# Kernel optimization log

Measured on AMD Instinct MI355X. Metric: run time of the kernel, lower is better.

The kernel has to match this reference:

```python
import jax, jax.numpy as jnp
import numpy as np

B, C, O, N, T, K = 4, 64, 64, 32768, 4, 9
PAD, DIL = 4, 1  # padding*dilation, dilation
SIGMA = 0.05
EPS_BN = 1e-5


def _gather_ch(x, idx):
    # x: [B, C, N], idx: [B, N] -> gather along last dim per channel
    idx3 = jnp.broadcast_to(idx[:, None, :], x.shape)
    return jnp.take_along_axis(x, idx3, axis=-1)


def _weighted_conv(x, coords, w):
    # x: [B,C,N], coords: [B,3,N], w: [O,C,K]
    xp = jnp.pad(x, ((0, 0), (0, 0), (PAD, PAD)))
    cp = jnp.pad(coords, ((0, 0), (0, 0), (PAD, PAD)))
    win_idx = jnp.arange(N)[:, None] + jnp.arange(K) * DIL  # [N, K]
    win = xp[:, :, win_idx]   # [B,C,N,K]
    cwin = cp[:, :, win_idx]  # [B,3,N,K]
    d = cwin - cwin[:, :, :, K // 2:K // 2 + 1]
    s = jnp.sum(d * d, axis=1)                    # [B,N,K]
    r = jnp.sqrt(jnp.where(s > 0, s, 1.0))
    r = jnp.where(s > 0, r, 0.0)
    wgt = jnp.maximum(1.0 - r / SIGMA, 0.0)       # [B,N,K]
    return jnp.einsum('bcnk,bnk,ock->bon', win, wgt, w)


def _bn(x, g, b):
    # training-mode BatchNorm1d over (B, N)
    m = jnp.mean(x, axis=(0, 2), keepdims=True)
    v = jnp.var(x, axis=(0, 2), keepdims=True)
    return g[None, :, None] * (x - m) * jax.lax.rsqrt(v + EPS_BN) + b[None, :, None]


def setup_inputs() -> dict:
    key = jax.random.key(0)
    ks = jax.random.split(key, 12)
    inp = jax.random.normal(ks[0], (B, C, N), dtype=jnp.float32)
    # coords in a small box so sigma=0.05 yields non-trivial weights
    multi_coords = jax.random.uniform(ks[1], (B, 3, N, T), dtype=jnp.float32) * 0.02
    indices = jax.random.randint(ks[2], (B, N, T), 0, N, dtype=jnp.int32)
    reindices = jax.random.randint(ks[3], (B, N, T), 0, N, dtype=jnp.int32)
    fan = C * K
    conv_w = jax.random.normal(ks[4], (T, O, C, K), dtype=jnp.float32) / np.sqrt(fan)
    bn_gamma = jnp.ones((T, O), dtype=jnp.float32)
    bn_beta = jnp.zeros((T, O), dtype=jnp.float32)
    fusion_w = jax.random.normal(ks[5], (O, T * O), dtype=jnp.float32) / np.sqrt(T * O)
    fusion_b = jnp.zeros((O,), dtype=jnp.float32)
    fusion_gamma = jnp.ones((O,), dtype=jnp.float32)
    fusion_beta = jnp.zeros((O,), dtype=jnp.float32)
    return {"input": inp, "multi_coords": multi_coords, "indices": indices,
            "reindices": reindices, "conv_w": conv_w, "bn_gamma": bn_gamma,
            "bn_beta": bn_beta, "fusion_w": fusion_w, "fusion_b": fusion_b,
            "fusion_gamma": fusion_gamma, "fusion_beta": fusion_beta}


def reference(input, multi_coords, indices, reindices, conv_w, bn_gamma, bn_beta,
              fusion_w, fusion_b, fusion_gamma, fusion_beta):
    outs = []
    for i in range(T):  # fixed small set of 4 Hilbert orders
        x = _gather_ch(input, indices[:, :, i])            # [B,C,N]
        x = _weighted_conv(x, multi_coords[:, :, :, i], conv_w[i])  # [B,O,N]
        x = _bn(x, bn_gamma[i], bn_beta[i])
        x = _gather_ch(x, reindices[:, :, i])
        outs.append(x)
    cat = jnp.concatenate(outs, axis=1)                    # [B, T*O, N]
    y = jnp.einsum('bcn,oc->bon', cat, fusion_w) + fusion_b[None, :, None]
    y = _bn(y, fusion_gamma, fusion_beta)
    return jax.nn.relu(y)
```

## Files before the change

kernel.cpp:

```cpp
#include <hip/hip_runtime.h>
#include <hip/hip_bf16.h>

#define BB 4
#define CC 64
#define OO 64
#define NN 32768
#define TT 4
#define KK 9
#define PADW 4
#define SIGMA 0.05f
#define EPS_BN 1e-5f

typedef __attribute__((ext_vector_type(8))) short bf16x8;
typedef __attribute__((ext_vector_type(4))) float f32x4;

__device__ __forceinline__ unsigned short f2bf(float f) {
  __hip_bfloat16 h = __float2bfloat16(f);
  return *reinterpret_cast<unsigned short*>(&h);
}
__device__ __forceinline__ float bf2f(unsigned short u) {
  unsigned int x = ((unsigned int)u) << 16;
  float f;
  __builtin_memcpy(&f, &x, 4);
  return f;
}
__device__ __forceinline__ unsigned int pkbf(float a, float b) {
  float2 t; t.x = a; t.y = b;
  __hip_bfloat162 h = __float22bfloat162_rn(t);
  unsigned int r;
  __builtin_memcpy(&r, &h, 4);
  return r;
}

__global__ __launch_bounds__(256) void transpose_kernel(
    const float* __restrict__ inp, unsigned short* __restrict__ xTb)
{
  const int n0 = blockIdx.x * 64;
  const int b  = blockIdx.y;
  const int tid = threadIdx.x;
  __shared__ float xt[64][65];
  {
    int nl = tid & 63, c4 = tid >> 6;
    #pragma unroll
    for (int i = 0; i < 16; ++i) {
      int c = c4 * 16 + i;
      xt[c][nl] = inp[((size_t)(b*CC + c))*NN + n0 + nl];
    }
  }
  __syncthreads();
  {
    int nl = tid >> 2, cq = tid & 3;
    unsigned int pk[8];
    #pragma unroll
    for (int i = 0; i < 8; ++i) {
      int c = cq*16 + i*2;
      pk[i] = pkbf(xt[c][nl], xt[c+1][nl]);
    }
    unsigned int* dst = (unsigned int*)(xTb + (((size_t)b*NN) + n0 + nl)*CC + cq*16);
    ((int4*)dst)[0] = make_int4((int)pk[0],(int)pk[1],(int)pk[2],(int)pk[3]);
    ((int4*)dst)[1] = make_int4((int)pk[4],(int)pk[5],(int)pk[6],(int)pk[7]);
  }
}

__global__ __launch_bounds__(256) void wprep_kernel(
    const float* __restrict__ cw, unsigned short* __restrict__ W4)
{
  const int k = blockIdx.x;
  const int t = blockIdx.y;
  for (int u = threadIdx.x; u < OO*CC; u += 256) {
    int o = u >> 6, c = u & 63;
    int ow = o >> 5, ot = (o >> 4) & 1, l15 = o & 15;
    int frag = c >> 5, q = (c >> 3) & 3, j = c & 7;
    float wv = cw[(((size_t)(t*OO + o))*CC + c)*KK + k];
    W4[(size_t)(t*9+k)*4096 + ow*2048 + ot*1024 + frag*512 + l15*32 + q*8 + j]
        = f2bf(wv);
  }
}

__global__ __launch_bounds__(256, 6) void conv_kernel(
    const unsigned short* __restrict__ xTb,
    const float* __restrict__ mc,
    const int*   __restrict__ ind,
    const unsigned short* __restrict__ W4,
    unsigned short* __restrict__ Y,
    float* __restrict__ cpart2)
{
  const int n0  = blockIdx.x * 128;
  const int b   = blockIdx.y;
  const int t   = blockIdx.z;
  const int tid = threadIdx.x;
  const int lane = tid & 63;
  const int w    = tid >> 6;
  const int l15  = lane & 15;
  const int q    = lane >> 4;
  const int ow   = w & 1;
  const int nw   = w >> 1;

  __shared__ short xg[136][72];
  __shared__ float wgl[128][10];
  __shared__ float mcs[3][140];

  int4 g[5];
  #pragma unroll
  for (int i = 0; i < 5; ++i) {
    int u = tid + 256*i;
    g[i] = make_int4(0,0,0,0);
    if (u < 1088) {
      int p = u >> 3, s = u & 7;
      int m = n0 + p - PADW;
      if (m >= 0 && m < NN) {
        int idx = ind[((size_t)b*NN + m)*TT + t];
        g[i] = *(const int4*)(xTb + ((size_t)b*NN + idx)*CC + s*8);
      }
    }
  }

  if (tid < 136) {
    int m = n0 + tid - PADW;
    #pragma unroll
    for (int d = 0; d < 3; ++d) {
      float4 v = make_float4(0.f, 0.f, 0.f, 0.f);
      if (m >= 0 && m < NN)
        v = *(const float4*)(mc + (((size_t)(b*3+d))*NN + m)*TT);
      mcs[d][tid] = (t==0) ? v.x : (t==1) ? v.y : (t==2) ? v.z : v.w;
    }
  }

  #pragma unroll
  for (int i = 0; i < 5; ++i) {
    int u = tid + 256*i;
    if (u < 1088) {
      int p = u >> 3, s = u & 7;
      *(int4*)&xg[p][s*8] = g[i];
    }
  }
  __syncthreads();

  {
    int nl = tid >> 1;
    int k0 = (tid & 1) * 5;
    int kc = 5 - (tid & 1);
    float cx = mcs[0][nl+4], cy = mcs[1][nl+4], cz = mcs[2][nl+4];
    for (int i2 = 0; i2 < kc; ++i2) {
      int k = k0 + i2, mi = nl + k;
      float dx = mcs[0][mi]-cx, dy = mcs[1][mi]-cy, dz = mcs[2][mi]-cz;
      float s2 = dx*dx + dy*dy + dz*dz;
      float r = (s2 > 0.f) ? sqrtf(s2) : 0.f;
      wgl[nl][k] = fmaxf(1.f - r*(1.f/SIGMA), 0.f);
    }
  }
  __syncthreads();

  const unsigned short* Wt = W4 + (size_t)t*9*4096 + ow*2048 + (l15*4 + q)*8;
  const f32x4 Z = {0.f, 0.f, 0.f, 0.f};
  f32x4 fin[2][4];
  #pragma unroll
  for (int ot = 0; ot < 2; ++ot)
    #pragma unroll
    for (int ns = 0; ns < 4; ++ns) fin[ot][ns] = Z;

  for (int k = 0; k < KK; ++k) {
    const unsigned short* Wk = Wt + (size_t)k*4096;
    bf16x8 af[2][2];
    #pragma unroll
    for (int ot = 0; ot < 2; ++ot) {
      af[ot][0] = *(const bf16x8*)(Wk + ot*1024);
      af[ot][1] = *(const bf16x8*)(Wk + ot*1024 + 512);
    }
    #pragma unroll
    for (int ns = 0; ns < 4; ++ns) {
      int nl = nw*64 + ns*16 + l15;
      int p  = nl + k;
      bf16x8 b0 = *(const bf16x8*)&xg[p][q*8];
      bf16x8 b1 = *(const bf16x8*)&xg[p][32 + q*8];
      float wgt = wgl[nl][k];
      #pragma unroll
      for (int ot = 0; ot < 2; ++ot) {
        f32x4 d = __builtin_amdgcn_mfma_f32_16x16x32_bf16(af[ot][0], b0, Z, 0, 0, 0);
        d = __builtin_amdgcn_mfma_f32_16x16x32_bf16(af[ot][1], b1, d, 0, 0, 0);
        fin[ot][ns] += wgt * d;
      }
    }
  }

  #pragma unroll
  for (int ns = 0; ns < 4; ++ns) {
    int nl = nw*64 + ns*16 + l15;
    size_t row = (((size_t)t*BB + b)*NN + n0 + nl)*OO;
    #pragma unroll
    for (int ot = 0; ot < 2; ++ot) {
      uint2 pk2;
      pk2.x = pkbf(fin[ot][ns][0], fin[ot][ns][1]);
      pk2.y = pkbf(fin[ot][ns][2], fin[ot][ns][3]);
      *(uint2*)(Y + row + ow*32 + ot*16 + q*4) = pk2;
    }
  }

  float sv[16];
  #pragma unroll
  for (int ot = 0; ot < 2; ++ot)
    #pragma unroll
    for (int r = 0; r < 4; ++r) {
      float a = 0.f, qs = 0.f;
      #pragma unroll
      for (int ns = 0; ns < 4; ++ns) {
        float v = fin[ot][ns][r];
        a += v; qs += v*v;
      }
      sv[ot*4+r] = a; sv[8+ot*4+r] = qs;
    }
  #pragma unroll
  for (int msk = 1; msk < 16; msk <<= 1) {
    #pragma unroll
    for (int i = 0; i < 16; ++i) sv[i] += __shfl_xor(sv[i], msk, 16);
  }
  if (l15 == 0) {
    int slot4 = ((b*256 + (int)blockIdx.x) << 2) | w;
    #pragma unroll
    for (int ot = 0; ot < 2; ++ot)
      #pragma unroll
      for (int r = 0; r < 4; ++r) {
        int o = ow*32 + ot*16 + q*4 + r;
        cpart2[((size_t)((t*64 + o)*2 + 0))*4096 + slot4] = sv[ot*4+r];
        cpart2[((size_t)((t*64 + o)*2 + 1))*4096 + slot4] = sv[8+ot*4+r];
      }
  }
}

__global__ __launch_bounds__(256) void bnparam_kernel(
    const float* __restrict__ cpart2,
    const float* __restrict__ gam,
    const float* __restrict__ bet,
    float* __restrict__ ss)
{
  const int to = blockIdx.x;
  const int tid = threadIdx.x;
  __shared__ float r1[256], r2[256];
  const float* p1 = cpart2 + (size_t)to*2*4096;
  const float* p2 = p1 + 4096;
  float s1 = 0.f, s2 = 0.f;
  for (int i = tid*4; i < 4096; i += 1024) {
    float4 a = *(const float4*)(p1 + i);
    float4 c = *(const float4*)(p2 + i);
    s1 += a.x + a.y + a.z + a.w;
    s2 += c.x + c.y + c.z + c.w;
  }
  r1[tid] = s1; r2[tid] = s2;
  __syncthreads();
  for (int st = 128; st > 0; st >>= 1) {
    if (tid < st) { r1[tid] += r1[tid+st]; r2[tid] += r2[tid+st]; }
    __syncthreads();
  }
  if (tid == 0) {
    const float inv = 1.f / (float)(BB * NN);
    float mean = r1[0] * inv;
    float var  = r2[0] * inv - mean * mean;
    float sc = gam[to] * rsqrtf(var + EPS_BN);
    ss[to*2 + 0] = sc;
    ss[to*2 + 1] = bet[to] - mean * sc;
  }
}

__global__ __launch_bounds__(256, 6) void fusion_kernel(
    const unsigned short* __restrict__ Y,
    const int*   __restrict__ rind,
    const float* __restrict__ ss,
    const float* __restrict__ fw,
    const float* __restrict__ fb,
    float* __restrict__ out,
    float* __restrict__ fpart2)
{
  const int n0  = blockIdx.x * 128;
  const int b   = blockIdx.y;
  const int tid = threadIdx.x;
  const int lane = tid & 63;
  const int w    = tid >> 6;
  const int l15  = lane & 15;
  const int q    = lane >> 4;
  const int ow   = w & 1;
  const int nw   = w >> 1;

  __shared__ short zg[128][72];
  __shared__ int   rnl[TT][128];
  __shared__ float ssl[512];

  for (int u = tid; u < 512; u += 256) {
    int tt = u >> 7, nl = u & 127;
    rnl[tt][nl] = rind[((size_t)b*NN + n0 + nl)*TT + tt];
  }
  ssl[tid]       = ss[tid];
  ssl[tid + 256] = ss[tid + 256];
  __syncthreads();

  f32x4 fin[2][4];
  #pragma unroll
  for (int ot = 0; ot < 2; ++ot)
    #pragma unroll
    for (int ns = 0; ns < 4; ++ns) fin[ot][ns] = (f32x4){0.f,0.f,0.f,0.f};

  for (int r = 0; r < 4; ++r) {
    if (r) __syncthreads();
    #pragma unroll
    for (int i = 0; i < 4; ++i) {
      int u = tid + 256*i;
      int n = u >> 3, s = u & 7;
      int rn = rnl[r][n];
      int4 raw = *(const int4*)(Y + (((size_t)r*BB + b)*NN + rn)*OO + s*8);
      const unsigned short* rp = (const unsigned short*)&raw;
      int cb = r*64 + s*8;
      unsigned int pk[4];
      #pragma unroll
      for (int j = 0; j < 4; ++j) {
        float v0 = bf2f(rp[2*j  ]) * ssl[(cb+2*j  )*2] + ssl[(cb+2*j  )*2+1];
        float v1 = bf2f(rp[2*j+1]) * ssl[(cb+2*j+1)*2] + ssl[(cb+2*j+1)*2+1];
        pk[j] = pkbf(v0, v1);
      }
      *(int4*)&zg[n][s*8] = make_int4((int)pk[0],(int)pk[1],(int)pk[2],(int)pk[3]);
    }
    __syncthreads();

    #pragma unroll
    for (int kk = 0; kk < 2; ++kk) {
      bf16x8 af[2];
      #pragma unroll
      for (int ot = 0; ot < 2; ++ot) {
        const float* wp = fw + (size_t)(ow*32 + ot*16 + l15)*256 + r*64 + kk*32 + q*8;
        float4 wa = *(const float4*)wp;
        float4 wb = *(const float4*)(wp + 4);
        unsigned int u0 = pkbf(wa.x, wa.y), u1 = pkbf(wa.z, wa.w);
        unsigned int u2 = pkbf(wb.x, wb.y), u3 = pkbf(wb.z, wb.w);
        int4 tmp = make_int4((int)u0,(int)u1,(int)u2,(int)u3);
        __builtin_memcpy(&af[ot], &tmp, 16);
      }
      #pragma unroll
      for (int ns = 0; ns < 4; ++ns) {
        int nl = nw*64 + ns*16 + l15;
        bf16x8 bfr = *(const bf16x8*)&zg[nl][kk*32 + q*8];
        #pragma unroll
        for (int ot = 0; ot < 2; ++ot)
          fin[ot][ns] = __builtin_amdgcn_mfma_f32_16x16x32_bf16(af[ot], bfr, fin[ot][ns], 0, 0, 0);
      }
    }
  }

  float sv[16];
  #pragma unroll
  for (int ot = 0; ot < 2; ++ot)
    #pragma unroll
    for (int rr = 0; rr < 4; ++rr) {
      int o = ow*32 + ot*16 + q*4 + rr;
      float bias = fb[o];
      float* dst = out + ((size_t)(b*OO + o))*NN + n0 + nw*64;
      float a = 0.f, qs = 0.f;
      #pragma unroll
      for (int ns = 0; ns < 4; ++ns) {
        float v = fin[ot][ns][rr] + bias;
        dst[ns*16 + l15] = v;
        a += v; qs += v*v;
      }
      sv[ot*4+rr] = a; sv[8+ot*4+rr] = qs;
    }
  #pragma unroll
  for (int msk = 1; msk < 16; msk <<= 1) {
    #pragma unroll
    for (int i = 0; i < 16; ++i) sv[i] += __shfl_xor(sv[i], msk, 16);
  }
  if (l15 == 0) {
    int slot4 = ((b*256 + (int)blockIdx.x) << 2) | w;
    #pragma unroll
    for (int ot = 0; ot < 2; ++ot)
      #pragma unroll
      for (int rr = 0; rr < 4; ++rr) {
        int o = ow*32 + ot*16 + q*4 + rr;
        fpart2[((size_t)(o*2 + 0))*4096 + slot4] = sv[ot*4+rr];
        fpart2[((size_t)(o*2 + 1))*4096 + slot4] = sv[8+ot*4+rr];
      }
  }
}

__global__ __launch_bounds__(256) void freduce_kernel(
    const float* __restrict__ fpart2,
    const float* __restrict__ fg,
    const float* __restrict__ fbeta,
    float* __restrict__ fss)
{
  const int o = blockIdx.x;
  const int tid = threadIdx.x;
  __shared__ float r1[256], r2[256];
  const float* p1 = fpart2 + (size_t)o*2*4096;
  const float* p2 = p1 + 4096;
  float s1 = 0.f, s2 = 0.f;
  for (int i = tid*4; i < 4096; i += 1024) {
    float4 a = *(const float4*)(p1 + i);
    float4 c = *(const float4*)(p2 + i);
    s1 += a.x + a.y + a.z + a.w;
    s2 += c.x + c.y + c.z + c.w;
  }
  r1[tid] = s1; r2[tid] = s2;
  __syncthreads();
  for (int st = 128; st > 0; st >>= 1) {
    if (tid < st) { r1[tid] += r1[tid+st]; r2[tid] += r2[tid+st]; }
    __syncthreads();
  }
  if (tid == 0) {
    const float inv = 1.f / (float)(BB * NN);
    float mean = r1[0] * inv;
    float var  = r2[0] * inv - mean * mean;
    float sc = fg[o] * rsqrtf(var + EPS_BN);
    fss[o*2 + 0] = sc;
    fss[o*2 + 1] = fbeta[o] - mean * sc;
  }
}

__global__ __launch_bounds__(256) void final_kernel(
    float* __restrict__ out, const float* __restrict__ fss)
{
  const int e0 = blockIdx.x * 2048 + threadIdx.x;
  #pragma unroll
  for (int s = 0; s < 8; ++s) {
    int e  = e0 + s * 256;
    int o2 = (e >> 15) & 63;
    float sc = fss[o2*2 + 0];
    float sh = fss[o2*2 + 1];
    float v = out[e] * sc + sh;
    out[e] = fmaxf(v, 0.f);
  }
}

extern "C" void kernel_launch(void* const* d_in, const int* in_sizes, int n_in,
                              void* d_out, int out_size, void* d_ws, size_t ws_size,
                              hipStream_t stream) {
  const float* inp  = (const float*)d_in[0];
  const float* mc   = (const float*)d_in[1];
  const int*   ind  = (const int*)  d_in[2];
  const int*   rind = (const int*)  d_in[3];
  const float* cw   = (const float*)d_in[4];
  const float* bg   = (const float*)d_in[5];
  const float* bb   = (const float*)d_in[6];
  const float* fw   = (const float*)d_in[7];
  const float* fb   = (const float*)d_in[8];
  const float* fg   = (const float*)d_in[9];
  const float* fbt  = (const float*)d_in[10];

  char* ws = (char*)d_ws;
  float* convss = (float*)(ws + 0);
  float* fss    = (float*)(ws + 2048);
  unsigned short* Y = (unsigned short*)(ws + 8192);
  float* fpart2 = (float*)(ws + 8192 + 33554432);

  char* ob = (char*)d_out;
  unsigned short* xTb = (unsigned short*)ob;
  unsigned short* W4  = (unsigned short*)(ob + 16777216);
  float*          cpart2 = (float*)(ob + 17072128);
  float* out = (float*)d_out;

  dim3 gt(NN/64, BB);
  transpose_kernel<<<gt, 256, 0, stream>>>(inp, xTb);

  dim3 gw(KK, TT);
  wprep_kernel<<<gw, 256, 0, stream>>>(cw, W4);

  dim3 gc(NN/128, BB, TT);
  conv_kernel<<<gc, 256, 0, stream>>>(xTb, mc, ind, W4, Y, cpart2);

  bnparam_kernel<<<256, 256, 0, stream>>>(cpart2, bg, bb, convss);

  dim3 gf(NN/128, BB);
  fusion_kernel<<<gf, 256, 0, stream>>>(Y, rind, convss, fw, fb, out, fpart2);

  freduce_kernel<<<OO, 256, 0, stream>>>(fpart2, fg, fbt, fss);

  final_kernel<<<(BB*OO*NN)/2048, 256, 0, stream>>>(out, fss);
}
```

Before: 262.0 us.

## Give each wave pair a private conv input tile and drop block barriers

The conv kernel now has each pair of waves that share an n-range gather its own 64-point halo tile, coordinates and weights into a private LDS slice. Each wave reads only data it wrote itself, so both __syncthreads are removed. The LDS tile drops its padded row layout in favour of an XOR swizzle to avoid bank conflicts. Launch bounds on the conv and fusion kernels drop from 6 to 4 blocks. In exchange, the two waves in a pair issue duplicate gather loads, the halo is re-fetched per 64 points, and register pressure rises with nine in-flight int4 loads per thread.

```diff
diff --git a/kernel.cpp b/kernel.cpp
--- a/kernel.cpp
+++ b/kernel.cpp
@@ -77,7 +77,7 @@
   }
 }
 
-__global__ __launch_bounds__(256, 6) void conv_kernel(
+__global__ __launch_bounds__(256, 4) void conv_kernel(
     const unsigned short* __restrict__ xTb,
     const float* __restrict__ mc,
     const int*   __restrict__ ind,
@@ -96,60 +96,55 @@
   const int ow   = w & 1;
   const int nw   = w >> 1;
 
-  __shared__ short xg[136][72];
-  __shared__ float wgl[128][10];
-  __shared__ float mcs[3][140];
-
-  int4 g[5];
-  #pragma unroll
-  for (int i = 0; i < 5; ++i) {
-    int u = tid + 256*i;
-    g[i] = make_int4(0,0,0,0);
-    if (u < 1088) {
-      int p = u >> 3, s = u & 7;
-      int m = n0 + p - PADW;
-      if (m >= 0 && m < NN) {
-        int idx = ind[((size_t)b*NN + m)*TT + t];
-        g[i] = *(const int4*)(xTb + ((size_t)b*NN + idx)*CC + s*8);
-      }
-    }
-  }
-
-  if (tid < 136) {
-    int m = n0 + tid - PADW;
+  __shared__ short xg[2][72*64];
+  __shared__ float wgl[2][64][10];
+  __shared__ float mcs[2][3][72];
+
+  const int nstart = n0 + nw*64;
+
+  for (int u = lane; u < 72; u += 64) {
+    int m = nstart + u - PADW;
     #pragma unroll
     for (int d = 0; d < 3; ++d) {
       float4 v = make_float4(0.f, 0.f, 0.f, 0.f);
       if (m >= 0 && m < NN)
         v = *(const float4*)(mc + (((size_t)(b*3+d))*NN + m)*TT);
-      mcs[d][tid] = (t==0) ? v.x : (t==1) ? v.y : (t==2) ? v.z : v.w;
-    }
-  }
-
-  #pragma unroll
-  for (int i = 0; i < 5; ++i) {
-    int u = tid + 256*i;
-    if (u < 1088) {
-      int p = u >> 3, s = u & 7;
-      *(int4*)&xg[p][s*8] = g[i];
-    }
-  }
-  __syncthreads();
+      mcs[nw][d][u] = (t==0) ? v.x : (t==1) ? v.y : (t==2) ? v.z : v.w;
+    }
+  }
+
+  int4 g[9];
+  #pragma unroll
+  for (int i = 0; i < 9; ++i) {
+    int u = lane + 64*i;
+    int p = u >> 3, s = u & 7;
+    int m = nstart + p - PADW;
+    g[i] = make_int4(0,0,0,0);
+    if (m >= 0 && m < NN) {
+      int idx = ind[((size_t)b*NN + m)*TT + t];
+      g[i] = *(const int4*)(xTb + ((size_t)b*NN + idx)*CC + s*8);
+    }
+  }
 
   {
-    int nl = tid >> 1;
-    int k0 = (tid & 1) * 5;
-    int kc = 5 - (tid & 1);
-    float cx = mcs[0][nl+4], cy = mcs[1][nl+4], cz = mcs[2][nl+4];
-    for (int i2 = 0; i2 < kc; ++i2) {
-      int k = k0 + i2, mi = nl + k;
-      float dx = mcs[0][mi]-cx, dy = mcs[1][mi]-cy, dz = mcs[2][mi]-cz;
+    int nl = lane;
+    float cx = mcs[nw][0][nl+4], cy = mcs[nw][1][nl+4], cz = mcs[nw][2][nl+4];
+    #pragma unroll
+    for (int k = 0; k < KK; ++k) {
+      float dx = mcs[nw][0][nl+k]-cx, dy = mcs[nw][1][nl+k]-cy, dz = mcs[nw][2][nl+k]-cz;
       float s2 = dx*dx + dy*dy + dz*dz;
       float r = (s2 > 0.f) ? sqrtf(s2) : 0.f;
-      wgl[nl][k] = fmaxf(1.f - r*(1.f/SIGMA), 0.f);
-    }
-  }
-  __syncthreads();
+      wgl[nw][nl][k] = fmaxf(1.f - r*(1.f/SIGMA), 0.f);
+    }
+  }
+
+  #pragma unroll
+  for (int i = 0; i < 9; ++i) {
+    int u = lane + 64*i;
+    int p = u >> 3, s = u & 7;
+    *(int4*)&xg[nw][p*64 + ((s ^ (p & 7)) << 3)] = g[i];
+  }
+  asm volatile("" ::: "memory");
 
   const unsigned short* Wt = W4 + (size_t)t*9*4096 + ow*2048 + (l15*4 + q)*8;
   const f32x4 Z = {0.f, 0.f, 0.f, 0.f};
@@ -169,11 +164,13 @@
     }
     #pragma unroll
     for (int ns = 0; ns < 4; ++ns) {
-      int nl = nw*64 + ns*16 + l15;
+      int nl = ns*16 + l15;
       int p  = nl + k;
-      bf16x8 b0 = *(const bf16x8*)&xg[p][q*8];
-      bf16x8 b1 = *(const bf16x8*)&xg[p][32 + q*8];
-      float wgt = wgl[nl][k];
+      const short* row = &xg[nw][p*64];
+      int sw = p & 7;
+      bf16x8 b0 = *(const bf16x8*)(row + ((q ^ sw) << 3));
+      bf16x8 b1 = *(const bf16x8*)(row + (((4 + q) ^ sw) << 3));
+      float wgt = wgl[nw][nl][k];
       #pragma unroll
       for (int ot = 0; ot < 2; ++ot) {
         f32x4 d = __builtin_amdgcn_mfma_f32_16x16x32_bf16(af[ot][0], b0, Z, 0, 0, 0);
@@ -261,7 +258,7 @@
   }
 }
 
-__global__ __launch_bounds__(256, 6) void fusion_kernel(
+__global__ __launch_bounds__(256, 4) void fusion_kernel(
     const unsigned short* __restrict__ Y,
     const int*   __restrict__ rind,
     const float* __restrict__ ss,
```

Result: faster. 230.1 us (-12.1%).
